# Optimization experiments

Measured on AMD Instinct MI355X. Metric: run time of the kernel, lower is better.

## Reference

```python
import jax, jax.numpy as jnp
import numpy as np
from jax import lax

G = 8  # number of RBF grid points (FastKAN default style)
GRID = jnp.linspace(-2.0, 2.0, G)
DENOM = 4.0 / (G - 1)  # grid spacing used as gaussian width


def _fastkan_conv(x, ln_w, ln_b, Wb, bb, Ws):
    # x: [B, C, H, W]; 3x3 conv, stride 1, pad 1 via patch unfold + FastKAN linear
    B, C, H, W = x.shape
    p = lax.conv_general_dilated_patches(x, (3, 3), (1, 1), ((1, 1), (1, 1)))  # [B, C*9, H, W]
    p = p.transpose(0, 2, 3, 1).reshape(B * H * W, C * 9)  # [N, in]
    # LayerNorm over patch features (FastKAN normalizes before the RBF basis)
    mu = p.mean(-1, keepdims=True)
    var = p.var(-1, keepdims=True)
    pn = (p - mu) / jnp.sqrt(var + 1e-5) * ln_w + ln_b
    # Gaussian RBF basis: [N, in, G]
    rbf = jnp.exp(-jnp.square((pn[:, :, None] - GRID) / DENOM))
    spline = rbf.reshape(B * H * W, -1) @ Ws.T          # [N, out]
    base = jax.nn.silu(p) @ Wb.T + bb                    # [N, out]
    out = spline + base
    return out.reshape(B, H, W, -1).transpose(0, 3, 1, 2)  # [B, out, H, W]


def _bn_relu_pool(h, gamma, beta):
    # BatchNorm2d in training mode (batch stats), ReLU, MaxPool2d(2,2)
    mu = h.mean((0, 2, 3), keepdims=True)
    var = h.var((0, 2, 3), keepdims=True)
    h = (h - mu) / jnp.sqrt(var + 1e-5) * gamma[None, :, None, None] + beta[None, :, None, None]
    h = jax.nn.relu(h)
    return lax.reduce_window(h, -jnp.inf, lax.max, (1, 1, 2, 2), (1, 1, 2, 2), 'VALID')


def setup_inputs() -> dict:
    key = jax.random.key(0)
    ks = jax.random.split(key, 16)
    B, Cin, H, W = 32, 16, 64, 64
    dims = [(Cin * 9, 64), (64 * 9, 128), (128 * 9, 256)]
    inp = {"x": jax.random.normal(ks[0], (B, Cin, H, W), jnp.float32)}
    for i, (fin, fout) in enumerate(dims, 1):
        inp[f"ln_w{i}"] = jnp.ones((fin,), jnp.float32)
        inp[f"ln_b{i}"] = jnp.zeros((fin,), jnp.float32)
        inp[f"Wb{i}"] = jax.random.normal(ks[3 * i], (fout, fin), jnp.float32) * 0.05
        inp[f"bb{i}"] = jnp.zeros((fout,), jnp.float32)
        inp[f"Ws{i}"] = jax.random.normal(ks[3 * i + 1], (fout, fin * G), jnp.float32) * 0.05
        inp[f"g{i}"] = jnp.ones((fout,), jnp.float32)
        inp[f"be{i}"] = jnp.zeros((fout,), jnp.float32)
    return inp


def reference(x, ln_w1, ln_b1, Wb1, bb1, Ws1, g1, be1,
              ln_w2, ln_b2, Wb2, bb2, Ws2, g2, be2,
              ln_w3, ln_b3, Wb3, bb3, Ws3, g3, be3):
    h = _bn_relu_pool(_fastkan_conv(x, ln_w1, ln_b1, Wb1, bb1, Ws1), g1, be1)
    h = _bn_relu_pool(_fastkan_conv(h, ln_w2, ln_b2, Wb2, bb2, Ws2), g2, be2)
    h = _bn_relu_pool(_fastkan_conv(h, ln_w3, ln_b3, Wb3, bb3, Ws3), g3, be3)
    return h.reshape(h.shape[0], -1)  # flatten: [B, 256*8*8]
```

## Files before the change

kernel.cpp:

```cpp
#include <hip/hip_runtime.h>

typedef _Float16 half_t;
typedef __attribute__((ext_vector_type(8))) _Float16 half8;
typedef __attribute__((ext_vector_type(4))) float floatx4;


#define RBF_SCALE 2.1019644f
#define RBF_G0   -4.2039288f
#define RBF_2D    2.40224482f
#define RBF_D2    1.44269504f
#define RBF_Q     0.13533528f
#define LOG2E     1.44269504f

template<int C, int HW>
__global__ __launch_bounds__(256)
void chan_ss(const float* __restrict__ src, float2* __restrict__ ss)
{
    int idx = blockIdx.x * 256 + threadIdx.x;
    int b = idx / HW, hw = idx - b * HW;
    const float* p = src + (long)b * C * HW + hw;
    float s = 0.f, s2 = 0.f;
    #pragma unroll 4
    for (int c = 0; c < C; ++c) {
        float v = p[(long)c * HW];
        s += v; s2 += v * v;
    }
    ss[idx] = make_float2(s, s2);
}

template<int IN, int H, int W>
__global__ __launch_bounds__(256)
void pix_stats(const float2* __restrict__ ss, float2* __restrict__ ms)
{
    const int HW = H * W;
    int idx = blockIdx.x * 256 + threadIdx.x;
    int b = idx / HW, hw = idx - b * HW;
    int h = hw / W, w = hw - h * W;
    float s = 0.f, s2 = 0.f;
    #pragma unroll
    for (int dy = -1; dy <= 1; ++dy)
        #pragma unroll
        for (int dx = -1; dx <= 1; ++dx) {
            int y = h + dy, xx = w + dx;
            if (y >= 0 && y < H && xx >= 0 && xx < W) {
                float2 v = ss[(long)b * HW + y * W + xx];
                s += v.x; s2 += v.y;
            }
        }
    float mean = s / IN;
    float istd = rsqrtf(s2 / IN - mean * mean + 1e-5f);
    ms[idx] = make_float2(mean, istd);
}

template<int C, int H, int W>
__global__ __launch_bounds__(256)
void ln_prep(const float* __restrict__ x,
             const float* __restrict__ lnw, const float* __restrict__ lnb,
             const float2* __restrict__ ms,
             half_t* __restrict__ pn, half_t* __restrict__ sp)
{
    const int HW = H * W, IN = C * 9;
    const int NL = (IN + 63) / 64;
    __shared__ float xw[C * 18];
    __shared__ short offs[C * 9];

    const int wv = threadIdx.x >> 6, lane = threadIdx.x & 63;
    const int pix0 = blockIdx.x * 4;
    const int b = pix0 / HW, hw0 = pix0 % HW;
    const int h = hw0 / W, x0 = hw0 % W;
    const float* xb = x + (long)b * C * HW;

    for (int idx = threadIdx.x; idx < C * 18; idx += 256) {
        int ch = idx / 18, rem = idx - ch * 18;
        int dy = rem / 6, dx = rem - dy * 6;
        int y = h + dy - 1, xx = x0 + dx - 1;
        float v = 0.f;
        if (y >= 0 && y < H && xx >= 0 && xx < W)
            v = xb[(long)ch * HW + y * W + xx];
        xw[idx] = v;
    }
    for (int i = threadIdx.x; i < IN; i += 256) {
        int ch = i / 9, r = i - ch * 9;
        int dy = r / 3, dx = r - dy * 3;
        offs[i] = (short)(ch * 18 + dy * 6 + dx);
    }
    __syncthreads();

    const int pix = pix0 + wv;
    float2 msv = ms[pix];
    const float mean = msv.x, istd = msv.y;

    #pragma unroll
    for (int t = 0; t < NL; ++t) {
        int i = t * 64 + lane;
        if (i < IN) {
            float val = xw[offs[i] + wv];
            float t0 = (val - mean) * istd;
            float pnv = fmaf(t0, lnw[i], lnb[i]) * RBF_SCALE;
            pnv = fminf(12.f, fmaxf(-12.f, pnv));
            pn[(long)pix * IN + i] = (half_t)pnv;
            float e = __builtin_amdgcn_exp2f(-val * LOG2E);
            sp[(long)pix * IN + i] = (half_t)(val * __builtin_amdgcn_rcpf(1.f + e));
        }
    }
}

template<int IN, int OUT>
__global__ __launch_bounds__(256)
void conv_w(const float* __restrict__ Ws, const float* __restrict__ Wb,
            half_t* __restrict__ Wt)
{
    const int NIB = (IN + 63) / 64, NSTEP = NIB * 9;
    int idx = blockIdx.x * 256 + threadIdx.x;
    if (idx >= OUT * NSTEP * 64) return;
    int uu = idx & 63;
    int t = idx >> 6;
    int o = t % OUT;
    int s = t / OUT;
    int iblk = s / 9, j = s % 9;
    int ulin = (((uu >> 3) ^ (o & 7)) << 3) + (uu & 7);
    int i = iblk * 64 + ulin;
    float v = 0.f;
    if (i < IN)
        v = (j < 8) ? Ws[(long)o * IN * 8 + i * 8 + j] : Wb[(long)o * IN + i];
    Wt[idx] = (half_t)v;
}

template<int IN, int OUT, int HW, int NB, int SPLIT>
__global__ __launch_bounds__(256)
void kan_gemm(const half_t* __restrict__ pn, const half_t* __restrict__ sp,
              const half_t* __restrict__ Wt, float* __restrict__ out)
{
    const int NIB = (IN + 63) / 64;

    __shared__ half_t As[64 * 64];
    __shared__ half_t Bs[NB * 64 * 64];

    const int tid = threadIdx.x;
    const int row = tid >> 2, q = tid & 3;
    const int pix = blockIdx.x * 64 + row;
    const half_t* pnrow = pn + (long)pix * IN;
    const half_t* sprow = sp + (long)pix * IN;

    const int wv = tid >> 6, lane = tid & 63;
    const int lr = lane & 15, lq = lane >> 4;
    const int u0 = (2 * q) ^ (row & 7);
    const int u1 = (2 * q + 1) ^ (row & 7);
    const int yoff = blockIdx.y * (4 * NB * 16);

    floatx4 acc[NB][4] = {};
    float r[16], u[16];
    half8 pf0, pf1;

    const int grpA = (blockIdx.z * NIB) / SPLIT;
    const int grpB = ((blockIdx.z + 1) * NIB) / SPLIT;
    const int s0 = grpA * 9, s1 = grpB * 9;

    int jg = 0, ibg = grpA;

    auto ldglob = [&](const half_t* base, int ib, half8& a, half8& b) {
        int i0 = ib * 64 + q * 16;
        const half_t* pp = base + ((i0 < IN) ? i0 : 0);
        a = *(const half8*)pp;
        b = *(const half8*)(pp + 8);
    };

    auto stageB = [&](int it) {
        const half_t* wsrc = Wt + (long)it * OUT * 64
                              + (long)(yoff + wv * NB * 16) * 64;
        #pragma unroll
        for (int c = 0; c < NB * 2; ++c) {
            __builtin_amdgcn_global_load_lds(
                (const __attribute__((address_space(1))) void*)(wsrc + c * 512 + lane * 8),
                (__attribute__((address_space(3))) void*)(&Bs[wv * NB * 1024 + c * 512]),
                16, 0, 0);
        }
    };

    auto genA = [&]() {
        if (jg < 8) {
            if (jg == 0) {
                #pragma unroll
                for (int kk = 0; kk < 8; ++kk) {
                    float d0 = (float)pf0[kk] - RBF_G0;
                    float d1 = (float)pf1[kk] - RBF_G0;
                    r[kk]     = __builtin_amdgcn_exp2f(-(d0 * d0));
                    u[kk]     = __builtin_amdgcn_exp2f(fmaf(RBF_2D, d0, -RBF_D2));
                    r[kk + 8] = __builtin_amdgcn_exp2f(-(d1 * d1));
                    u[kk + 8] = __builtin_amdgcn_exp2f(fmaf(RBF_2D, d1, -RBF_D2));
                }
            }
            half8 a0, a1;
            #pragma unroll
            for (int kk = 0; kk < 8; ++kk) {
                a0[kk] = (half_t)r[kk];
                a1[kk] = (half_t)r[kk + 8];
            }
            *(half8*)&As[row * 64 + u0 * 8] = a0;
            *(half8*)&As[row * 64 + u1 * 8] = a1;
            if (jg < 7) {
                #pragma unroll
                for (int kk = 0; kk < 16; ++kk) { r[kk] *= u[kk]; u[kk] *= RBF_Q; }
            }
            if (jg == 7) ldglob(sprow, ibg, pf0, pf1);
        } else {
            *(half8*)&As[row * 64 + u0 * 8] = pf0;
            *(half8*)&As[row * 64 + u1 * 8] = pf1;
            ldglob(pnrow, ibg + 1, pf0, pf1);
        }
        if (++jg == 9) { jg = 0; ++ibg; }
    };

    auto domfma = [&]() {
        __builtin_amdgcn_s_setprio(1);
        #pragma unroll
        for (int ks = 0; ks < 2; ++ks) {
            half8 af[4], bf[NB];
            #pragma unroll
            for (int mf = 0; mf < 4; ++mf) {
                int rr = mf * 16 + lr;
                af[mf] = *(const half8*)&As[rr * 64 + (((ks * 4 + lq) ^ (rr & 7)) * 8)];
            }
            #pragma unroll
            for (int nb = 0; nb < NB; ++nb) {
                int rr = wv * NB * 16 + nb * 16 + lr;
                bf[nb] = *(const half8*)&Bs[rr * 64 + (((ks * 4 + lq) ^ (rr & 7)) * 8)];
            }
            #pragma unroll
            for (int nb = 0; nb < NB; ++nb)
                #pragma unroll
                for (int mf = 0; mf < 4; ++mf)
                    acc[nb][mf] = __builtin_amdgcn_mfma_f32_16x16x32_f16(
                        bf[nb], af[mf], acc[nb][mf], 0, 0, 0);
        }
        __builtin_amdgcn_s_setprio(0);
    };

    ldglob(pnrow, grpA, pf0, pf1);

    for (int it = s0; it < s1; ++it) {
        __syncthreads();
        stageB(it);
        genA();
        __syncthreads();
        domfma();
    }

    const long zoff = (long)blockIdx.z * ((long)gridDim.x * 64) * OUT;
    #pragma unroll
    for (int nb = 0; nb < NB; ++nb)
    #pragma unroll
    for (int mf = 0; mf < 4; ++mf)
    #pragma unroll
    for (int reg = 0; reg < 4; ++reg) {
        int o  = yoff + wv * NB * 16 + nb * 16 + lq * 4 + reg;
        int p2 = blockIdx.x * 64 + mf * 16 + lr;
        int b2 = p2 / HW, hw2 = p2 % HW;
        out[zoff + ((long)b2 * OUT + o) * HW + hw2] = acc[nb][mf][reg];
    }
}

__launch_bounds__(256)
__global__ void bn_stats(const float* __restrict__ h, const float* __restrict__ bias,
                         int C, int HW, int B, int nz, float* __restrict__ sums)
{
    int c = blockIdx.y;
    float bbc = bias[c];
    long zstride = (long)B * C * HW;
    int total = B * HW;
    float s = 0.f, s2 = 0.f;
    for (int idx = blockIdx.x * 256 + threadIdx.x; idx < total; idx += 256 * gridDim.x) {
        int b = idx / HW, r = idx % HW;
        long base = ((long)b * C + c) * HW + r;
        float v = bbc;
        for (int z = 0; z < nz; ++z) v += h[z * zstride + base];
        s += v; s2 += v * v;
    }
    for (int off = 32; off > 0; off >>= 1) {
        s  += __shfl_down(s,  off, 64);
        s2 += __shfl_down(s2, off, 64);
    }
    __shared__ float rs[4], rs2[4];
    int lane = threadIdx.x & 63, wid = threadIdx.x >> 6;
    if (lane == 0) { rs[wid] = s; rs2[wid] = s2; }
    __syncthreads();
    if (threadIdx.x == 0) {
        atomicAdd(&sums[c],     rs[0] + rs[1] + rs[2] + rs[3]);
        atomicAdd(&sums[C + c], rs2[0] + rs2[1] + rs2[2] + rs2[3]);
    }
}

__launch_bounds__(256)
__global__ void bn_relu_pool(const float* __restrict__ h, const float* __restrict__ sums,
                             const float* __restrict__ bias,
                             const float* __restrict__ gamma, const float* __restrict__ beta,
                             float* __restrict__ out, int B, int C, int H, int W, int nz)
{
    int Ho = H / 2, Wo = W / 2;
    long total = (long)B * C * Ho * Wo;
    long idx = (long)blockIdx.x * 256 + threadIdx.x;
    if (idx >= total) return;
    int pw = idx % Wo; long t = idx / Wo;
    int ph = t % Ho; t /= Ho;
    int c = t % C; int b = (int)(t / C);

    float M = (float)B * H * W;
    float mean = sums[c] / M;
    float var  = sums[C + c] / M - mean * mean;
    float scale = gamma[c] * rsqrtf(var + 1e-5f);
    float shift = beta[c] - mean * scale + bias[c] * scale;

    long zstride = (long)B * C * H * W;
    const float* hp = h + ((long)b * C + c) * H * W;
    float m = 0.f;
    #pragma unroll
    for (int i = 0; i < 2; ++i)
        #pragma unroll
        for (int j = 0; j < 2; ++j) {
            long off = (2 * ph + i) * W + 2 * pw + j;
            float v = 0.f;
            for (int z = 0; z < nz; ++z) v += hp[z * zstride + off];
            v = v * scale + shift;
            m = fmaxf(m, v);
        }
    out[idx] = m;
}

extern "C" void kernel_launch(void* const* d_in, const int* in_sizes, int n_in,
                              void* d_out, int out_size, void* d_ws, size_t ws_size,
                              hipStream_t stream) {
    const float* x     = (const float*)d_in[0];
    const float* ln_w1 = (const float*)d_in[1];  const float* ln_b1 = (const float*)d_in[2];
    const float* Wb1   = (const float*)d_in[3];  const float* bb1   = (const float*)d_in[4];
    const float* Ws1   = (const float*)d_in[5];  const float* g1    = (const float*)d_in[6];
    const float* be1   = (const float*)d_in[7];
    const float* ln_w2 = (const float*)d_in[8];  const float* ln_b2 = (const float*)d_in[9];
    const float* Wb2   = (const float*)d_in[10]; const float* bb2   = (const float*)d_in[11];
    const float* Ws2   = (const float*)d_in[12]; const float* g2    = (const float*)d_in[13];
    const float* be2   = (const float*)d_in[14];
    const float* ln_w3 = (const float*)d_in[15]; const float* ln_b3 = (const float*)d_in[16];
    const float* Wb3   = (const float*)d_in[17]; const float* bb3   = (const float*)d_in[18];
    const float* Ws3   = (const float*)d_in[19]; const float* g3    = (const float*)d_in[20];
    const float* be3   = (const float*)d_in[21];

    const int B = 32;
    char* ws = (char*)d_ws;
    float*  convbuf = (float*)(ws + 0);
    float2* ssbuf   = (float2*)(ws + 0);
    float2* msbuf   = (float2*)(ws + 1048576);
    float*  poolbuf = (float*)(ws + 33554432);
    float*  stats1  = (float*)(ws + 41943040);
    float*  stats2  = (float*)(ws + 41945088);
    float*  stats3  = (float*)(ws + 41947136);
    half_t* wt1     = (half_t*)(ws + 41949184);
    half_t* wt2     = (half_t*)(ws + 42170368);
    half_t* wt3     = (half_t*)(ws + 43497472);
    half_t* pnbuf   = (half_t*)(ws + 48805888);
    half_t* spbuf   = (half_t*)(ws + 86554624);

    hipMemsetAsync(stats1, 0, 6144, stream);

    conv_w<144, 64><<<(64 * 27 * 64 + 255) / 256, 256, 0, stream>>>(Ws1, Wb1, wt1);
    conv_w<576, 128><<<(128 * 81 * 64 + 255) / 256, 256, 0, stream>>>(Ws2, Wb2, wt2);
    conv_w<1152, 256><<<(256 * 162 * 64 + 255) / 256, 256, 0, stream>>>(Ws3, Wb3, wt3);

    {
        const int H = 64, W = 64, OUT = 64;
        int npix = B * H * W;
        chan_ss<16, H * W><<<npix / 256, 256, 0, stream>>>(x, ssbuf);
        pix_stats<144, H, W><<<npix / 256, 256, 0, stream>>>(ssbuf, msbuf);
        ln_prep<16, H, W><<<npix / 4, 256, 0, stream>>>(x, ln_w1, ln_b1, msbuf, pnbuf, spbuf);
        kan_gemm<144, OUT, H * W, 1, 1><<<dim3(npix / 64, 1, 1), 256, 0, stream>>>(
            pnbuf, spbuf, wt1, convbuf);
        bn_stats<<<dim3(64, OUT), 256, 0, stream>>>(convbuf, bb1, OUT, H * W, B, 1, stats1);
        long tot = (long)B * OUT * (H / 2) * (W / 2);
        bn_relu_pool<<<(tot + 255) / 256, 256, 0, stream>>>(
            convbuf, stats1, bb1, g1, be1, poolbuf, B, OUT, H, W, 1);
    }
    {
        const int H = 32, W = 32, OUT = 128;
        int npix = B * H * W;
        chan_ss<64, H * W><<<npix / 256, 256, 0, stream>>>(poolbuf, ssbuf);
        pix_stats<576, H, W><<<npix / 256, 256, 0, stream>>>(ssbuf, msbuf);
        ln_prep<64, H, W><<<npix / 4, 256, 0, stream>>>(poolbuf, ln_w2, ln_b2, msbuf, pnbuf, spbuf);
        kan_gemm<576, OUT, H * W, 2, 2><<<dim3(npix / 64, 1, 2), 256, 0, stream>>>(
            pnbuf, spbuf, wt2, convbuf);
        bn_stats<<<dim3(16, OUT), 256, 0, stream>>>(convbuf, bb2, OUT, H * W, B, 2, stats2);
        long tot = (long)B * OUT * (H / 2) * (W / 2);
        bn_relu_pool<<<(tot + 255) / 256, 256, 0, stream>>>(
            convbuf, stats2, bb2, g2, be2, poolbuf, B, OUT, H, W, 2);
    }
    {
        const int H = 16, W = 16, OUT = 256;
        int npix = B * H * W;
        chan_ss<128, H * W><<<npix / 256, 256, 0, stream>>>(poolbuf, ssbuf);
        pix_stats<1152, H, W><<<npix / 256, 256, 0, stream>>>(ssbuf, msbuf);
        ln_prep<128, H, W><<<npix / 4, 256, 0, stream>>>(poolbuf, ln_w3, ln_b3, msbuf, pnbuf, spbuf);
        kan_gemm<1152, OUT, H * W, 2, 4><<<dim3(npix / 64, 2, 4), 256, 0, stream>>>(
            pnbuf, spbuf, wt3, convbuf);
        bn_stats<<<dim3(8, OUT), 256, 0, stream>>>(convbuf, bb3, OUT, H * W, B, 4, stats3);
        long tot = (long)B * OUT * (H / 2) * (W / 2);
        bn_relu_pool<<<(tot + 255) / 256, 256, 0, stream>>>(
            convbuf, stats3, bb3, g3, be3, (float*)d_out, B, OUT, H, W, 4);
    }
}
```

Measured before the change: 481.3 us.

## Fuse LayerNorm and SiLU into GEMM A-tile generation, store raw fp16 im2col once

The prep kernel no longer writes two fp16 buffers (normalized values and SiLU values). It now writes a single raw im2col buffer, 16 pixels per block with a wider shared window. The GEMM applies the per-pixel mean/istd and the LN affine when generating the RBF tiles, and computes SiLU on the fly for the base tile. This halves the intermediate write and read traffic but adds ALU work and ln_w/ln_b loads inside the GEMM. Rounding the raw values to fp16 before normalization also changes precision slightly.

```diff
diff --git a/kernel.cpp b/kernel.cpp
--- a/kernel.cpp
+++ b/kernel.cpp
@@ -54,53 +54,48 @@
 
 template<int C, int H, int W>
 __global__ __launch_bounds__(256)
-void ln_prep(const float* __restrict__ x,
-             const float* __restrict__ lnw, const float* __restrict__ lnb,
-             const float2* __restrict__ ms,
-             half_t* __restrict__ pn, half_t* __restrict__ sp)
+void im2col(const float* __restrict__ x, half_t* __restrict__ val)
 {
     const int HW = H * W, IN = C * 9;
     const int NL = (IN + 63) / 64;
-    __shared__ float xw[C * 18];
-    __shared__ short offs[C * 9];
+    __shared__ float xw[C * 57];
 
     const int wv = threadIdx.x >> 6, lane = threadIdx.x & 63;
-    const int pix0 = blockIdx.x * 4;
+    const int pix0 = blockIdx.x * 16;
     const int b = pix0 / HW, hw0 = pix0 % HW;
     const int h = hw0 / W, x0 = hw0 % W;
     const float* xb = x + (long)b * C * HW;
 
-    for (int idx = threadIdx.x; idx < C * 18; idx += 256) {
-        int ch = idx / 18, rem = idx - ch * 18;
-        int dy = rem / 6, dx = rem - dy * 6;
-        int y = h + dy - 1, xx = x0 + dx - 1;
+    for (int idx = threadIdx.x; idx < C * 54; idx += 256) {
+        int ch = idx / 54, rem = idx - ch * 54;
+        int dy = rem / 18, col = rem - dy * 18;
+        int y = h + dy - 1, xx = x0 + col - 1;
         float v = 0.f;
         if (y >= 0 && y < H && xx >= 0 && xx < W)
             v = xb[(long)ch * HW + y * W + xx];
-        xw[idx] = v;
-    }
-    for (int i = threadIdx.x; i < IN; i += 256) {
-        int ch = i / 9, r = i - ch * 9;
-        int dy = r / 3, dx = r - dy * 3;
-        offs[i] = (short)(ch * 18 + dy * 6 + dx);
+        xw[ch * 57 + dy * 19 + col] = v;
     }
     __syncthreads();
 
-    const int pix = pix0 + wv;
-    float2 msv = ms[pix];
-    const float mean = msv.x, istd = msv.y;
-
+    int ga[NL];
     #pragma unroll
     for (int t = 0; t < NL; ++t) {
         int i = t * 64 + lane;
         if (i < IN) {
-            float val = xw[offs[i] + wv];
-            float t0 = (val - mean) * istd;
-            float pnv = fmaf(t0, lnw[i], lnb[i]) * RBF_SCALE;
-            pnv = fminf(12.f, fmaxf(-12.f, pnv));
-            pn[(long)pix * IN + i] = (half_t)pnv;
-            float e = __builtin_amdgcn_exp2f(-val * LOG2E);
-            sp[(long)pix * IN + i] = (half_t)(val * __builtin_amdgcn_rcpf(1.f + e));
+            int ch = i / 9, r = i - ch * 9;
+            int dy = r / 3, dx = r - dy * 3;
+            ga[t] = ch * 57 + dy * 19 + dx;
+        } else ga[t] = 0;
+    }
+
+    #pragma unroll
+    for (int p = 0; p < 4; ++p) {
+        const int px = wv * 4 + p;
+        const long base = (long)(pix0 + px) * IN;
+        #pragma unroll
+        for (int t = 0; t < NL; ++t) {
+            int i = t * 64 + lane;
+            if (i < IN) val[base + i] = (half_t)xw[ga[t] + px];
         }
     }
 }
@@ -128,7 +123,8 @@
 
 template<int IN, int OUT, int HW, int NB, int SPLIT>
 __global__ __launch_bounds__(256)
-void kan_gemm(const half_t* __restrict__ pn, const half_t* __restrict__ sp,
+void kan_gemm(const half_t* __restrict__ val, const float2* __restrict__ ms,
+              const float* __restrict__ lnw, const float* __restrict__ lnb,
               const half_t* __restrict__ Wt, float* __restrict__ out)
 {
     const int NIB = (IN + 63) / 64;
@@ -139,8 +135,7 @@
     const int tid = threadIdx.x;
     const int row = tid >> 2, q = tid & 3;
     const int pix = blockIdx.x * 64 + row;
-    const half_t* pnrow = pn + (long)pix * IN;
-    const half_t* sprow = sp + (long)pix * IN;
+    const half_t* valrow = val + (long)pix * IN;
 
     const int wv = tid >> 6, lane = tid & 63;
     const int lr = lane & 15, lq = lane >> 4;
@@ -148,6 +143,9 @@
     const int u1 = (2 * q + 1) ^ (row & 7);
     const int yoff = blockIdx.y * (4 * NB * 16);
 
+    const float2 msv = ms[pix];
+    const float mean = msv.x, istd = msv.y;
+
     floatx4 acc[NB][4] = {};
     float r[16], u[16];
     half8 pf0, pf1;
@@ -158,11 +156,11 @@
 
     int jg = 0, ibg = grpA;
 
-    auto ldglob = [&](const half_t* base, int ib, half8& a, half8& b) {
+    auto ldglob = [&](int ib) {
         int i0 = ib * 64 + q * 16;
-        const half_t* pp = base + ((i0 < IN) ? i0 : 0);
-        a = *(const half8*)pp;
-        b = *(const half8*)(pp + 8);
+        const half_t* pp = valrow + ((i0 < IN) ? i0 : 0);
+        pf0 = *(const half8*)pp;
+        pf1 = *(const half8*)(pp + 8);
     };
 
     auto stageB = [&](int it) {
@@ -180,12 +178,30 @@
     auto genA = [&]() {
         if (jg < 8) {
             if (jg == 0) {
+                int i0c = ibg * 64 + q * 16;
+                int ic = (i0c < IN) ? i0c : 0;
+                const float4* lwp = (const float4*)(lnw + ic);
+                const float4* lbp = (const float4*)(lnb + ic);
+                float lw[8], lb[8];
+                *(float4*)&lw[0] = lwp[0]; *(float4*)&lw[4] = lwp[1];
+                *(float4*)&lb[0] = lbp[0]; *(float4*)&lb[4] = lbp[1];
                 #pragma unroll
                 for (int kk = 0; kk < 8; ++kk) {
-                    float d0 = (float)pf0[kk] - RBF_G0;
-                    float d1 = (float)pf1[kk] - RBF_G0;
-                    r[kk]     = __builtin_amdgcn_exp2f(-(d0 * d0));
-                    u[kk]     = __builtin_amdgcn_exp2f(fmaf(RBF_2D, d0, -RBF_D2));
+                    float v0 = (float)pf0[kk];
+                    float pnv = fmaf((v0 - mean) * istd, lw[kk], lb[kk]) * RBF_SCALE;
+                    pnv = fminf(12.f, fmaxf(-12.f, pnv));
+                    float d0 = pnv - RBF_G0;
+                    r[kk] = __builtin_amdgcn_exp2f(-(d0 * d0));
+                    u[kk] = __builtin_amdgcn_exp2f(fmaf(RBF_2D, d0, -RBF_D2));
+                }
+                *(float4*)&lw[0] = lwp[2]; *(float4*)&lw[4] = lwp[3];
+                *(float4*)&lb[0] = lbp[2]; *(float4*)&lb[4] = lbp[3];
+                #pragma unroll
+                for (int kk = 0; kk < 8; ++kk) {
+                    float v1 = (float)pf1[kk];
+                    float pnv = fmaf((v1 - mean) * istd, lw[kk], lb[kk]) * RBF_SCALE;
+                    pnv = fminf(12.f, fmaxf(-12.f, pnv));
+                    float d1 = pnv - RBF_G0;
                     r[kk + 8] = __builtin_amdgcn_exp2f(-(d1 * d1));
                     u[kk + 8] = __builtin_amdgcn_exp2f(fmaf(RBF_2D, d1, -RBF_D2));
                 }
@@ -202,11 +218,21 @@
                 #pragma unroll
                 for (int kk = 0; kk < 16; ++kk) { r[kk] *= u[kk]; u[kk] *= RBF_Q; }
             }
-            if (jg == 7) ldglob(sprow, ibg, pf0, pf1);
+            if (jg == 7) ldglob(ibg);
         } else {
-            *(half8*)&As[row * 64 + u0 * 8] = pf0;
-            *(half8*)&As[row * 64 + u1 * 8] = pf1;
-            ldglob(pnrow, ibg + 1, pf0, pf1);
+            half8 a0, a1;
+            #pragma unroll
+            for (int kk = 0; kk < 8; ++kk) {
+                float v0 = (float)pf0[kk];
+                float v1 = (float)pf1[kk];
+                a0[kk] = (half_t)(v0 * __builtin_amdgcn_rcpf(
+                             1.f + __builtin_amdgcn_exp2f(-v0 * LOG2E)));
+                a1[kk] = (half_t)(v1 * __builtin_amdgcn_rcpf(
+                             1.f + __builtin_amdgcn_exp2f(-v1 * LOG2E)));
+            }
+            *(half8*)&As[row * 64 + u0 * 8] = a0;
+            *(half8*)&As[row * 64 + u1 * 8] = a1;
+            ldglob(ibg + 1);
         }
         if (++jg == 9) { jg = 0; ++ibg; }
     };
@@ -236,7 +262,7 @@
         __builtin_amdgcn_s_setprio(0);
     };
 
-    ldglob(pnrow, grpA, pf0, pf1);
+    ldglob(grpA);
 
     for (int it = s0; it < s1; ++it) {
         __syncthreads();
@@ -346,8 +372,6 @@
     const int B = 32;
     char* ws = (char*)d_ws;
     float*  convbuf = (float*)(ws + 0);
-    float2* ssbuf   = (float2*)(ws + 0);
-    float2* msbuf   = (float2*)(ws + 1048576);
     float*  poolbuf = (float*)(ws + 33554432);
     float*  stats1  = (float*)(ws + 41943040);
     float*  stats2  = (float*)(ws + 41945088);
@@ -355,8 +379,9 @@
     half_t* wt1     = (half_t*)(ws + 41949184);
     half_t* wt2     = (half_t*)(ws + 42170368);
     half_t* wt3     = (half_t*)(ws + 43497472);
-    half_t* pnbuf   = (half_t*)(ws + 48805888);
-    half_t* spbuf   = (half_t*)(ws + 86554624);
+    half_t* valbuf  = (half_t*)(ws + 48805888);
+    float2* ssbuf   = (float2*)(ws + 86554624);
+    float2* msbuf   = (float2*)(ws + 87603200);
 
     hipMemsetAsync(stats1, 0, 6144, stream);
 
@@ -369,9 +394,9 @@
         int npix = B * H * W;
         chan_ss<16, H * W><<<npix / 256, 256, 0, stream>>>(x, ssbuf);
         pix_stats<144, H, W><<<npix / 256, 256, 0, stream>>>(ssbuf, msbuf);
-        ln_prep<16, H, W><<<npix / 4, 256, 0, stream>>>(x, ln_w1, ln_b1, msbuf, pnbuf, spbuf);
+        im2col<16, H, W><<<npix / 16, 256, 0, stream>>>(x, valbuf);
         kan_gemm<144, OUT, H * W, 1, 1><<<dim3(npix / 64, 1, 1), 256, 0, stream>>>(
-            pnbuf, spbuf, wt1, convbuf);
+            valbuf, msbuf, ln_w1, ln_b1, wt1, convbuf);
         bn_stats<<<dim3(64, OUT), 256, 0, stream>>>(convbuf, bb1, OUT, H * W, B, 1, stats1);
         long tot = (long)B * OUT * (H / 2) * (W / 2);
         bn_relu_pool<<<(tot + 255) / 256, 256, 0, stream>>>(
@@ -382,9 +407,9 @@
         int npix = B * H * W;
         chan_ss<64, H * W><<<npix / 256, 256, 0, stream>>>(poolbuf, ssbuf);
         pix_stats<576, H, W><<<npix / 256, 256, 0, stream>>>(ssbuf, msbuf);
-        ln_prep<64, H, W><<<npix / 4, 256, 0, stream>>>(poolbuf, ln_w2, ln_b2, msbuf, pnbuf, spbuf);
+        im2col<64, H, W><<<npix / 16, 256, 0, stream>>>(poolbuf, valbuf);
         kan_gemm<576, OUT, H * W, 2, 2><<<dim3(npix / 64, 1, 2), 256, 0, stream>>>(
-            pnbuf, spbuf, wt2, convbuf);
+            valbuf, msbuf, ln_w2, ln_b2, wt2, convbuf);
         bn_stats<<<dim3(16, OUT), 256, 0, stream>>>(convbuf, bb2, OUT, H * W, B, 2, stats2);
         long tot = (long)B * OUT * (H / 2) * (W / 2);
         bn_relu_pool<<<(tot + 255) / 256, 256, 0, stream>>>(
@@ -395,9 +420,9 @@
         int npix = B * H * W;
         chan_ss<128, H * W><<<npix / 256, 256, 0, stream>>>(poolbuf, ssbuf);
         pix_stats<1152, H, W><<<npix / 256, 256, 0, stream>>>(ssbuf, msbuf);
-        ln_prep<128, H, W><<<npix / 4, 256, 0, stream>>>(poolbuf, ln_w3, ln_b3, msbuf, pnbuf, spbuf);
+        im2col<128, H, W><<<npix / 16, 256, 0, stream>>>(poolbuf, valbuf);
         kan_gemm<1152, OUT, H * W, 2, 4><<<dim3(npix / 64, 2, 4), 256, 0, stream>>>(
-            pnbuf, spbuf, wt3, convbuf);
+            valbuf, msbuf, ln_w3, ln_b3, wt3, convbuf);
         bn_stats<<<dim3(8, OUT), 256, 0, stream>>>(convbuf, bb3, OUT, H * W, B, 4, stats3);
         long tot = (long)B * OUT * (H / 2) * (W / 2);
         bn_relu_pool<<<(tot + 255) / 256, 256, 0, stream>>>(
```

After: 471.8 us. -2.0%, faster.
